# Kernel tuning notes

Hardware: AMD Instinct MI355X
Metric: run time of the kernel (lower is better)

Reference implementation:

```python
import jax, jax.numpy as jnp
import numpy as np

B, C, H, W = 16, 8, 512, 512
NUM_BINS = 15
NW = 3  # neighborhood_width
NORMALIZE = True


def setup_inputs() -> dict:
    key = jax.random.key(0)
    k1, k2 = jax.random.split(key)
    logits = jax.random.normal(k1, (B, C, H, W), dtype=jnp.float32)
    # calibration table: [num_classes, nw^2 neighbor counts, num conf bins]
    val_freqs = jax.random.uniform(k2, (C, NW * NW, NUM_BINS), dtype=jnp.float32)
    return {"logits": logits, "val_freqs": val_freqs}


def _count_matching_neighbors(onehot):
    # onehot: [B,C,H,W] binary (1 where argmax == class c). For each pixel count
    # neighbors in the NWxNW window sharing its binary value, excluding the center.
    kernel = jnp.ones((C, 1, NW, NW), onehot.dtype)
    conv = lambda x: jax.lax.conv_general_dilated(
        x, kernel, window_strides=(1, 1), padding='SAME', feature_group_count=C,
        dimension_numbers=('NCHW', 'OIHW', 'NCHW'))
    same_if_one = conv(onehot)          # matches when center==1
    same_if_zero = conv(1.0 - onehot)   # matches when center==0
    cnt = onehot * same_if_one + (1.0 - onehot) * same_if_zero - 1.0  # drop self-match
    return jnp.clip(cnt, 0, NW * NW - 1).astype(jnp.int32)


def reference(logits, val_freqs):
    probs = jax.nn.softmax(logits, axis=1)                  # [B,C,H,W]
    hard_pred = jnp.argmax(probs, axis=1)                   # [B,H,W]
    onehot = jax.nn.one_hot(hard_pred, C, axis=1, dtype=probs.dtype)  # [B,C,H,W]
    nn_cnt = _count_matching_neighbors(onehot)              # [B,C,H,W] int32 in [0, NW^2-1]
    # uniform bins on [0,1): bin = clip(floor(p * num_bins), 0, num_bins-1)
    bin_idx = jnp.clip(jnp.floor(probs * NUM_BINS).astype(jnp.int32), 0, NUM_BINS - 1)
    c_idx = jnp.arange(C)[None, :, None, None]              # broadcast class index
    calibrated = val_freqs[c_idx, nn_cnt, bin_idx]          # gather from calib table
    if NORMALIZE:
        calibrated = calibrated / jnp.sum(calibrated, axis=1, keepdims=True)
    return calibrated
```

## Files before the change

kernel.cpp:

```cpp
#include <hip/hip_runtime.h>
#include <cmath>

#define CC_ 8
#define HH 512
#define WW 512
#define TW 32
#define TH 32
#define OHS 35
#define NWG ((WW/TW)*(HH/TH)*16)
#define LOG2E 1.44269504088896340736f

typedef float vfloat4 __attribute__((ext_vector_type(4)));

__device__ __forceinline__ float comp4(const float4 v, int i){
  return (i==0)?v.x:((i==1)?v.y:((i==2)?v.z:v.w));
}

__device__ __forceinline__ void px_bins(const float* l, unsigned int& bw_out, int& pc_out){
  float e[CC_]; float S = 0.f;
  #pragma unroll
  for (int c = 0; c < CC_; ++c){
    e[c] = __builtin_amdgcn_exp2f(l[c] * LOG2E);
    S += e[c];
  }
  float b1 = e[0], b2 = 0.f; int pc = 0;
  #pragma unroll
  for (int c = 1; c < CC_; ++c){
    bool gt = e[c] > b1;
    b2 = gt ? b1 : fmaxf(b2, e[c]);
    pc = gt ? c : pc;
    b1 = gt ? e[c] : b1;
  }
  float r15 = 15.0f * __builtin_amdgcn_rcpf(S);
  unsigned int bw = 0;
  bool bad = (b1 - b2) < 1e-5f * b1;
  #pragma unroll
  for (int c = 0; c < CC_; ++c){
    float t = e[c] * r15;
    float rn = rintf(t);
    bad = bad || (rn > 0.5f && fabsf(t - rn) < 1e-4f);
    int b = (int)t; b = b > 14 ? 14 : b;
    bw |= (unsigned)b << (4*c);
  }
  if (bad){
    float m = l[0];
    #pragma unroll
    for (int c = 1; c < CC_; ++c) m = fmaxf(m, l[c]);
    float ee[CC_]; float SS = 0.f;
    #pragma unroll
    for (int c = 0; c < CC_; ++c){ ee[c] = expf(l[c]-m); SS += ee[c]; }
    float p[CC_];
    #pragma unroll
    for (int c = 0; c < CC_; ++c) p[c] = ee[c]/SS;
    float best = p[0]; pc = 0;
    #pragma unroll
    for (int c = 1; c < CC_; ++c){ if (p[c] > best){ best = p[c]; pc = c; } }
    bw = 0;
    #pragma unroll
    for (int c = 0; c < CC_; ++c){
      int b = (int)(p[c]*15.0f); b = b > 14 ? 14 : b;
      bw |= (unsigned)b << (4*c);
    }
  }
  bw_out = bw; pc_out = pc;
}

__global__ __launch_bounds__(256, 4) void nectar_binning_kernel(
    const float* __restrict__ logits,
    const float* __restrict__ vf,
    float* __restrict__ out){
  __shared__ float s_vf[CC_*144];
  __shared__ unsigned int s_oneh[(TH+2)*OHS];

  const int tid = threadIdx.x;

  const int lin  = blockIdx.x;
  const int virt = (lin & 7) * (NWG/8) + (lin >> 3);
  const int bz   = virt >> 8;
  const int rem  = virt & 255;
  const int h0   = (rem >> 4) * TH;
  const int w0   = (rem & 15) * TW;
  const long base_b = (long)bz * (CC_*HH*WW);

  const int tx = tid & 7;
  const int ty = tid >> 3;

  const int gw = w0 + 4*tx;
  const int gh = h0 + ty;
  const float* lp = logits + base_b + (long)gh*WW + gw;
  float4 lv[CC_];
  #pragma unroll
  for (int c = 0; c < CC_; ++c) lv[c] = *reinterpret_cast<const float4*>(lp + (long)c*(HH*WW));

  float hl[CC_]; bool hval = false; int hr = 0, hc = 0;
  if (tid < 132){
    int r, c;
    if      (tid < 34){ r = -1;       c = tid - 1;  }
    else if (tid < 68){ r = TH;       c = tid - 35; }
    else if (tid < 100){ r = tid-68;  c = -1;       }
    else               { r = tid-100; c = TW;       }
    hr = r; hc = c;
    const int hh = h0 + r, ww = w0 + c;
    hval = (hh >= 0 && hh < HH && ww >= 0 && ww < WW);
    const int hhc = min(max(hh,0),HH-1), wwc = min(max(ww,0),WW-1);
    const float* hp = logits + base_b + (long)hhc*WW + wwc;
    #pragma unroll
    for (int c2 = 0; c2 < CC_; ++c2) hl[c2] = hp[(long)c2*(HH*WW)];
  }

  for (int i = tid; i < CC_*9*15; i += 256){
    int b = i % 15, q = i / 15;
    int nn = q % 9, c = q / 9;
    s_vf[c*144 + b*9 + nn] = vf[i];
  }

  unsigned int binw[4];

  #pragma unroll
  for (int i = 0; i < 4; ++i){
    float l[CC_];
    #pragma unroll
    for (int c = 0; c < CC_; ++c) l[c] = comp4(lv[c], i);
    int pc; px_bins(l, binw[i], pc);
    s_oneh[(ty+1)*OHS + 4*tx + i + 1] = 1u << (4*pc);
  }

  if (tid < 132){
    unsigned int oh = 0u;
    if (hval){
      float b1 = hl[0], b2 = -1e30f; int pc = 0;
      #pragma unroll
      for (int c2 = 1; c2 < CC_; ++c2){
        bool gt = hl[c2] > b1;
        b2 = gt ? b1 : fmaxf(b2, hl[c2]);
        pc = gt ? c2 : pc;
        b1 = gt ? hl[c2] : b1;
      }
      if (b1 - b2 < 1e-5f){
        float e[CC_]; float S = 0.f;
        #pragma unroll
        for (int c2 = 0; c2 < CC_; ++c2){ e[c2] = expf(hl[c2]-b1); S += e[c2]; }
        float p[CC_];
        #pragma unroll
        for (int c2 = 0; c2 < CC_; ++c2) p[c2] = e[c2]/S;
        float best = p[0]; pc = 0;
        #pragma unroll
        for (int c2 = 1; c2 < CC_; ++c2){ if (p[c2] > best){ best = p[c2]; pc = c2; } }
      }
      oh = 1u << (4*pc);
    }
    s_oneh[(hr+1)*OHS + hc + 1] = oh;
  }

  __syncthreads();

  unsigned int cs[6];
  #pragma unroll
  for (int kk = 0; kk < 6; ++kk){
    int cidx = 4*tx + kk;
    cs[kk] = s_oneh[ ty   *OHS + cidx]
           + s_oneh[(ty+1)*OHS + cidx]
           + s_oneh[(ty+2)*OHS + cidx];
  }
  float4 o[CC_];
  #pragma unroll
  for (int i = 0; i < 4; ++i){
    unsigned int ctr = s_oneh[(ty+1)*OHS + 4*tx + i + 1];
    unsigned int acc = cs[i] + cs[i+1] + cs[i+2] - ctr;
    unsigned int valid = (acc * 0x11111111u) >> 28;
    unsigned int bw = binw[i];
    float v[CC_]; float S2 = 0.f;
    #pragma unroll
    for (int c = 0; c < CC_; ++c){
      unsigned int nc = (acc >> (4*c)) & 0xFu;
      unsigned int nn = ((ctr >> (4*c)) & 1u) ? nc : (valid - nc);
      unsigned int b  = (bw  >> (4*c)) & 0xFu;
      float t = s_vf[c*144 + b*9 + nn];
      v[c] = t; S2 += t;
    }
    float r2 = 1.0f / S2;
    #pragma unroll
    for (int c = 0; c < CC_; ++c){
      float res = v[c]*r2;
      if(i==0) o[c].x = res; else if(i==1) o[c].y = res; else if(i==2) o[c].z = res; else o[c].w = res;
    }
  }
  #pragma unroll
  for (int c = 0; c < CC_; ++c){
    vfloat4 nv = { o[c].x, o[c].y, o[c].z, o[c].w };
    __builtin_nontemporal_store(nv,
      reinterpret_cast<vfloat4*>(out + base_b + (long)c*(HH*WW) + (long)gh*WW + gw));
  }
}

extern "C" void kernel_launch(void* const* d_in, const int* in_sizes, int n_in,
                              void* d_out, int out_size, void* d_ws, size_t ws_size,
                              hipStream_t stream){
  const float* logits = (const float*)d_in[0];
  const float* vf     = (const float*)d_in[1];
  float* out          = (float*)d_out;
  nectar_binning_kernel<<<dim3(NWG), 256, 0, stream>>>(logits, vf, out);
}
```

Before: 51.76 us.

## Process two batch tiles per workgroup with software-pipelined loads

Each workgroup now handles the same spatial tile for two batch images (b and b+8), halving the grid to 2048 workgroups. The second image's logits are loaded while the first is being binned and written out, which should hide memory latency and amortize the calibration-table staging into shared memory. In exchange it raises register pressure from holding two sets of float4 loads, and it lowers the number of workgroups available to fill the GPU.

```diff
diff --git a/kernel.cpp b/kernel.cpp
--- a/kernel.cpp
+++ b/kernel.cpp
@@ -7,7 +7,7 @@
 #define TW 32
 #define TH 32
 #define OHS 35
-#define NWG ((WW/TW)*(HH/TH)*16)
+#define NWG 2048
 #define LOG2E 1.44269504088896340736f
 
 typedef float vfloat4 __attribute__((ext_vector_type(4)));
@@ -65,34 +65,100 @@
   bw_out = bw; pc_out = pc;
 }
 
+__device__ __forceinline__ int halo_argmax(const float* hl){
+  float b1 = hl[0], b2 = -1e30f; int pc = 0;
+  #pragma unroll
+  for (int c2 = 1; c2 < CC_; ++c2){
+    bool gt = hl[c2] > b1;
+    b2 = gt ? b1 : fmaxf(b2, hl[c2]);
+    pc = gt ? c2 : pc;
+    b1 = gt ? hl[c2] : b1;
+  }
+  if (b1 - b2 < 1e-5f){
+    float e[CC_]; float S = 0.f;
+    #pragma unroll
+    for (int c2 = 0; c2 < CC_; ++c2){ e[c2] = expf(hl[c2]-b1); S += e[c2]; }
+    float p[CC_];
+    #pragma unroll
+    for (int c2 = 0; c2 < CC_; ++c2) p[c2] = e[c2]/S;
+    float best = p[0]; pc = 0;
+    #pragma unroll
+    for (int c2 = 1; c2 < CC_; ++c2){ if (p[c2] > best){ best = p[c2]; pc = c2; } }
+  }
+  return pc;
+}
+
+__device__ __forceinline__ void epilogue(const unsigned int* oneh, const float* s_vf,
+                                         const unsigned int* binw, float* op,
+                                         int tx, int ty){
+  unsigned int cs[6];
+  #pragma unroll
+  for (int kk = 0; kk < 6; ++kk){
+    int cidx = 4*tx + kk;
+    cs[kk] = oneh[ ty   *OHS + cidx]
+           + oneh[(ty+1)*OHS + cidx]
+           + oneh[(ty+2)*OHS + cidx];
+  }
+  float4 o[CC_];
+  #pragma unroll
+  for (int i = 0; i < 4; ++i){
+    unsigned int ctr = oneh[(ty+1)*OHS + 4*tx + i + 1];
+    unsigned int acc = cs[i] + cs[i+1] + cs[i+2] - ctr;
+    unsigned int valid = (acc * 0x11111111u) >> 28;
+    unsigned int bw = binw[i];
+    float v[CC_]; float S2 = 0.f;
+    #pragma unroll
+    for (int c = 0; c < CC_; ++c){
+      unsigned int nc = (acc >> (4*c)) & 0xFu;
+      unsigned int nn = ((ctr >> (4*c)) & 1u) ? nc : (valid - nc);
+      unsigned int b  = (bw  >> (4*c)) & 0xFu;
+      float t = s_vf[c*144 + b*9 + nn];
+      v[c] = t; S2 += t;
+    }
+    float r2 = 1.0f / S2;
+    #pragma unroll
+    for (int c = 0; c < CC_; ++c){
+      float res = v[c]*r2;
+      if(i==0) o[c].x = res; else if(i==1) o[c].y = res; else if(i==2) o[c].z = res; else o[c].w = res;
+    }
+  }
+  #pragma unroll
+  for (int c = 0; c < CC_; ++c){
+    vfloat4 nv = { o[c].x, o[c].y, o[c].z, o[c].w };
+    __builtin_nontemporal_store(nv, reinterpret_cast<vfloat4*>(op + (long)c*(HH*WW)));
+  }
+}
+
 __global__ __launch_bounds__(256, 4) void nectar_binning_kernel(
     const float* __restrict__ logits,
     const float* __restrict__ vf,
     float* __restrict__ out){
   __shared__ float s_vf[CC_*144];
-  __shared__ unsigned int s_oneh[(TH+2)*OHS];
+  __shared__ unsigned int s_oneh[2][(TH+2)*OHS];
 
   const int tid = threadIdx.x;
 
   const int lin  = blockIdx.x;
   const int virt = (lin & 7) * (NWG/8) + (lin >> 3);
-  const int bz   = virt >> 8;
+  const int pz   = virt >> 8;
   const int rem  = virt & 255;
   const int h0   = (rem >> 4) * TH;
   const int w0   = (rem & 15) * TW;
-  const long base_b = (long)bz * (CC_*HH*WW);
+  const long base1 = (long)pz * (CC_*HH*WW);
+  const long base2 = base1 + (long)8 * (CC_*HH*WW);
 
   const int tx = tid & 7;
   const int ty = tid >> 3;
-
   const int gw = w0 + 4*tx;
   const int gh = h0 + ty;
-  const float* lp = logits + base_b + (long)gh*WW + gw;
-  float4 lv[CC_];
-  #pragma unroll
-  for (int c = 0; c < CC_; ++c) lv[c] = *reinterpret_cast<const float4*>(lp + (long)c*(HH*WW));
-
-  float hl[CC_]; bool hval = false; int hr = 0, hc = 0;
+  const long int_off = (long)gh*WW + gw;
+
+  const float* lp1 = logits + base1 + int_off;
+  float4 lv1[CC_];
+  #pragma unroll
+  for (int c = 0; c < CC_; ++c) lv1[c] = *reinterpret_cast<const float4*>(lp1 + (long)c*(HH*WW));
+
+  bool hval = false; int hr = 0, hc = 0; long hoff = 0;
   if (tid < 132){
     int r, c;
     if      (tid < 34){ r = -1;       c = tid - 1;  }
@@ -102,10 +168,13 @@
     hr = r; hc = c;
     const int hh = h0 + r, ww = w0 + c;
     hval = (hh >= 0 && hh < HH && ww >= 0 && ww < WW);
-    const int hhc = min(max(hh,0),HH-1), wwc = min(max(ww,0),WW-1);
-    const float* hp = logits + base_b + (long)hhc*WW + wwc;
-    #pragma unroll
-    for (int c2 = 0; c2 < CC_; ++c2) hl[c2] = hp[(long)c2*(HH*WW)];
+    hoff = (long)min(max(hh,0),HH-1)*WW + min(max(ww,0),WW-1);
+  }
+  float hl1[CC_];
+  if (tid < 132){
+    const float* hp = logits + base1 + hoff;
+    #pragma unroll
+    for (int c2 = 0; c2 < CC_; ++c2) hl1[c2] = hp[(long)c2*(HH*WW)];
   }
 
   for (int i = tid; i < CC_*9*15; i += 256){
@@ -114,83 +183,50 @@
     s_vf[c*144 + b*9 + nn] = vf[i];
   }
 
-  unsigned int binw[4];
-
+  unsigned int binw1[4];
   #pragma unroll
   for (int i = 0; i < 4; ++i){
     float l[CC_];
     #pragma unroll
-    for (int c = 0; c < CC_; ++c) l[c] = comp4(lv[c], i);
-    int pc; px_bins(l, binw[i], pc);
-    s_oneh[(ty+1)*OHS + 4*tx + i + 1] = 1u << (4*pc);
-  }
-
+    for (int c = 0; c < CC_; ++c) l[c] = comp4(lv1[c], i);
+    int pc; px_bins(l, binw1[i], pc);
+    s_oneh[0][(ty+1)*OHS + 4*tx + i + 1] = 1u << (4*pc);
+  }
+
+  const float* lp2 = logits + base2 + int_off;
+  float4 lv2[CC_];
+  #pragma unroll
+  for (int c = 0; c < CC_; ++c) lv2[c] = *reinterpret_cast<const float4*>(lp2 + (long)c*(HH*WW));
+  float hl2[CC_];
   if (tid < 132){
-    unsigned int oh = 0u;
-    if (hval){
-      float b1 = hl[0], b2 = -1e30f; int pc = 0;
-      #pragma unroll
-      for (int c2 = 1; c2 < CC_; ++c2){
-        bool gt = hl[c2] > b1;
-        b2 = gt ? b1 : fmaxf(b2, hl[c2]);
-        pc = gt ? c2 : pc;
-        b1 = gt ? hl[c2] : b1;
-      }
-      if (b1 - b2 < 1e-5f){
-        float e[CC_]; float S = 0.f;
-        #pragma unroll
-        for (int c2 = 0; c2 < CC_; ++c2){ e[c2] = expf(hl[c2]-b1); S += e[c2]; }
-        float p[CC_];
-        #pragma unroll
-        for (int c2 = 0; c2 < CC_; ++c2) p[c2] = e[c2]/S;
-        float best = p[0]; pc = 0;
-        #pragma unroll
-        for (int c2 = 1; c2 < CC_; ++c2){ if (p[c2] > best){ best = p[c2]; pc = c2; } }
-      }
-      oh = 1u << (4*pc);
-    }
-    s_oneh[(hr+1)*OHS + hc + 1] = oh;
-  }
+    const float* hp = logits + base2 + hoff;
+    #pragma unroll
+    for (int c2 = 0; c2 < CC_; ++c2) hl2[c2] = hp[(long)c2*(HH*WW)];
+  }
+
+  if (tid < 132)
+    s_oneh[0][(hr+1)*OHS + hc + 1] = hval ? (1u << (4*halo_argmax(hl1))) : 0u;
 
   __syncthreads();
 
-  unsigned int cs[6];
-  #pragma unroll
-  for (int kk = 0; kk < 6; ++kk){
-    int cidx = 4*tx + kk;
-    cs[kk] = s_oneh[ ty   *OHS + cidx]
-           + s_oneh[(ty+1)*OHS + cidx]
-           + s_oneh[(ty+2)*OHS + cidx];
-  }
-  float4 o[CC_];
+  epilogue(s_oneh[0], s_vf, binw1, out + base1 + int_off, tx, ty);
+
+  unsigned int binw2[4];
   #pragma unroll
   for (int i = 0; i < 4; ++i){
-    unsigned int ctr = s_oneh[(ty+1)*OHS + 4*tx + i + 1];
-    unsigned int acc = cs[i] + cs[i+1] + cs[i+2] - ctr;
-    unsigned int valid = (acc * 0x11111111u) >> 28;
-    unsigned int bw = binw[i];
-    float v[CC_]; float S2 = 0.f;
-    #pragma unroll
-    for (int c = 0; c < CC_; ++c){
-      unsigned int nc = (acc >> (4*c)) & 0xFu;
-      unsigned int nn = ((ctr >> (4*c)) & 1u) ? nc : (valid - nc);
-      unsigned int b  = (bw  >> (4*c)) & 0xFu;
-      float t = s_vf[c*144 + b*9 + nn];
-      v[c] = t; S2 += t;
-    }
-    float r2 = 1.0f / S2;
-    #pragma unroll
-    for (int c = 0; c < CC_; ++c){
-      float res = v[c]*r2;
-      if(i==0) o[c].x = res; else if(i==1) o[c].y = res; else if(i==2) o[c].z = res; else o[c].w = res;
-    }
-  }
-  #pragma unroll
-  for (int c = 0; c < CC_; ++c){
-    vfloat4 nv = { o[c].x, o[c].y, o[c].z, o[c].w };
-    __builtin_nontemporal_store(nv,
-      reinterpret_cast<vfloat4*>(out + base_b + (long)c*(HH*WW) + (long)gh*WW + gw));
-  }
+    float l[CC_];
+    #pragma unroll
+    for (int c = 0; c < CC_; ++c) l[c] = comp4(lv2[c], i);
+    int pc; px_bins(l, binw2[i], pc);
+    s_oneh[1][(ty+1)*OHS + 4*tx + i + 1] = 1u << (4*pc);
+  }
+
+  if (tid < 132)
+    s_oneh[1][(hr+1)*OHS + hc + 1] = hval ? (1u << (4*halo_argmax(hl2))) : 0u;
+
+  __syncthreads();
+
+  epilogue(s_oneh[1], s_vf, binw2, out + base2 + int_off, tx, ty);
 }
 
 extern "C" void kernel_launch(void* const* d_in, const int* in_sizes, int n_in,
```

Result: no change. 52.35 us (+1.1%).
